# Optimization experiments

Measured on AMD Instinct MI355X. Metric: run time of the kernel, lower is better.

The kernel has to match this reference:

```python
import jax, jax.numpy as jnp
import numpy as np

NEG_SLOPE = 0.2


def setup_inputs() -> dict:
    key = jax.random.key(0)
    k1, k2, k3 = jax.random.split(key, 3)
    B, N, IN, OUT, C = 2048, 256, 256, 256, 1024
    x = jax.random.normal(k1, (B, N, IN), dtype=jnp.float32)
    indices = jax.random.randint(k2, (B,), 0, C)
    # kaiming-uniform-like init for weight
    bound = float(np.sqrt(6.0 / IN))
    weight = jax.random.uniform(k3, (C, IN, OUT), dtype=jnp.float32, minval=-bound, maxval=bound)
    bias = jnp.zeros((1, 1, OUT), dtype=jnp.float32)
    return {"x": x, "indices": indices, "weight": weight, "bias": bias}


def reference(x, indices, weight, bias):
    # gather per-batch weight tiles: [B, IN, OUT], then batched matmul
    w = weight[indices]                      # [B, IN, OUT]
    out = jnp.einsum('bni,bio->bno', x, w)   # [B, N, OUT]
    out = out + bias[0]                      # bias[0] is [1, OUT], broadcasts
    return jnp.where(out >= 0, out, NEG_SLOPE * out)  # LeakyReLU(0.2)
```

## Files before the change

kernel.cpp:

```cpp
#include <hip/hip_runtime.h>
#include <hip/hip_bf16.h>


#define N_DIM 256
#define K_DIM 256
#define O_DIM 256
#define BK 32

typedef __attribute__((ext_vector_type(8))) __bf16 bf16x8;
typedef __attribute__((ext_vector_type(4))) float f32x4;
typedef __attribute__((ext_vector_type(4))) unsigned int u32x4;
typedef __attribute__((ext_vector_type(2))) unsigned int u32x2;

__device__ __forceinline__ f32x4 MFMA(u32x4 a, u32x4 b, f32x4 c) {
    return __builtin_amdgcn_mfma_f32_16x16x32_bf16(
        __builtin_bit_cast(bf16x8, a), __builtin_bit_cast(bf16x8, b), c, 0, 0, 0);
}

__device__ __forceinline__ unsigned pk2(float a, float b) {
    __hip_bfloat16 ha = __float2bfloat16(a);
    __hip_bfloat16 hb = __float2bfloat16(b);
    unsigned short sa, sb;
    __builtin_memcpy(&sa, &ha, 2);
    __builtin_memcpy(&sb, &hb, 2);
    return (unsigned)sa | ((unsigned)sb << 16);
}

__device__ __forceinline__ int swz(int row, int k) {
    const int rp = row >> 1;
    const int ch = (((row & 1) << 2) + (k >> 3)) ^ (rp & 7);
    return rp * 128 + ch * 16 + (k & 7) * 2;
}

__global__ __launch_bounds__(256) void argemm_kernel(
    const float* __restrict__ x,
    const int* __restrict__ idx,
    const float* __restrict__ w,
    const float* __restrict__ bias,
    float* __restrict__ out)
{
    __shared__ __align__(16) char lds[32768];

    const int tid = threadIdx.x;
    const int l   = tid & 63;
    const int wid = tid >> 6;
    const int wr  = wid >> 1;
    const int wc  = wid & 1;

    const unsigned bid     = blockIdx.x;
    const unsigned chunk   = gridDim.x >> 3;
    const unsigned logical = (bid & 7u) * chunk + (bid >> 3);
    const int b    = (int)(logical >> 2);
    const int tpos = (int)(logical & 3u);
    const int n0   = (tpos >> 1) * 128;
    const int o0   = (tpos & 1) * 128;

    const int c = idx[b];
    const float* xb = x + (size_t)b * (N_DIM * K_DIM);
    const float* wb = w + (size_t)c * (K_DIM * O_DIM);

    const int lr3 = l >> 3, kc = l & 7;
    int gA[4], aW[4];
#pragma unroll
    for (int q = 0; q < 4; ++q) {
        const int rA = wid * 32 + q * 8 + lr3;
        gA[q] = (n0 + rA) * K_DIM + kc * 4;
        aW[q] = swz(rA, kc * 4);
    }
    const int kq = tid >> 5;
    const int m4 = (tid & 31) * 4;
    int gB[4], bW[4];
#pragma unroll
    for (int dk = 0; dk < 4; ++dk)
        gB[dk] = (kq * 4 + dk) * O_DIM + o0 + m4;
#pragma unroll
    for (int j = 0; j < 4; ++j)
        bW[j] = 16384 + swz(m4 + j, kq * 4);

    const int g = l >> 4;
    const int i = l & 15;
    int aR[4], bR[4];
#pragma unroll
    for (int m = 0; m < 4; ++m) aR[m] = swz(wr * 64 + m * 16 + i, g * 8);
#pragma unroll
    for (int n = 0; n < 4; ++n) bR[n] = 16384 + swz(wc * 64 + n * 16 + i, g * 8);

    f32x4 ra[4], rb[4];

    auto issue = [&](int t) {
#pragma unroll
        for (int q = 0; q < 4; ++q)
            ra[q] = *(const f32x4*)(xb + gA[q] + t * BK);
#pragma unroll
        for (int dk = 0; dk < 4; ++dk)
            rb[dk] = *(const f32x4*)(wb + gB[dk] + t * (BK * O_DIM));
    };
    auto flush = [&](int buf) {
        char* base = (char*)lds + buf * 8192;
#pragma unroll
        for (int q = 0; q < 4; ++q) {
            u32x2 p;
            p.x = pk2(ra[q].x, ra[q].y);
            p.y = pk2(ra[q].z, ra[q].w);
            *(u32x2*)(base + aW[q]) = p;
        }
#pragma unroll
        for (int j = 0; j < 4; ++j) {
            u32x2 p;
            p.x = pk2(rb[0][j], rb[1][j]);
            p.y = pk2(rb[2][j], rb[3][j]);
            *(u32x2*)(base + bW[j]) = p;
        }
    };

    f32x4 acc[4][4];
#pragma unroll
    for (int m = 0; m < 4; ++m)
#pragma unroll
        for (int n = 0; n < 4; ++n)
            acc[m][n] = (f32x4){0.f, 0.f, 0.f, 0.f};

    issue(0);
    flush(0);
    issue(1);
    asm volatile("s_waitcnt lgkmcnt(0)" ::: "memory");
    __builtin_amdgcn_sched_barrier(0);
    __builtin_amdgcn_s_barrier();

#pragma unroll
    for (int t = 0; t < 8; ++t) {
        const int cur = t & 1;
        const char* base = (const char*)lds + cur * 8192;

        u32x4 af[4];
#pragma unroll
        for (int m = 0; m < 4; ++m)
            af[m] = *(const u32x4*)(base + aR[m]);
#pragma unroll
        for (int n = 0; n < 4; ++n) {
            const u32x4 bq = *(const u32x4*)(base + bR[n]);
#pragma unroll
            for (int m = 0; m < 4; ++m)
                acc[m][n] = MFMA(af[m], bq, acc[m][n]);
        }

        if (t < 7) {
            flush(cur ^ 1);
            if (t < 6) issue(t + 2);
            asm volatile("s_waitcnt lgkmcnt(0)" ::: "memory");
            __builtin_amdgcn_sched_barrier(0);
            __builtin_amdgcn_s_barrier();
        }
    }

    float biasf[4];
#pragma unroll
    for (int n = 0; n < 4; ++n)
        biasf[n] = bias[o0 + wc * 64 + n * 16 + i];

    float* ob = out + (size_t)b * (N_DIM * O_DIM);
#pragma unroll
    for (int m = 0; m < 4; ++m) {
#pragma unroll
        for (int r = 0; r < 4; ++r) {
            const int row = n0 + wr * 64 + m * 16 + g * 4 + r;
#pragma unroll
            for (int n = 0; n < 4; ++n) {
                float v = acc[m][n][r] + biasf[n];
                v = (v >= 0.f) ? v : 0.2f * v;
                ob[row * O_DIM + o0 + wc * 64 + n * 16 + i] = v;
            }
        }
    }
}

extern "C" void kernel_launch(void* const* d_in, const int* in_sizes, int n_in,
                              void* d_out, int out_size, void* d_ws, size_t ws_size,
                              hipStream_t stream) {
    const float* x    = (const float*)d_in[0];
    const int*   idx  = (const int*)d_in[1];
    const float* w    = (const float*)d_in[2];
    const float* bias = (const float*)d_in[3];
    float*       out  = (float*)d_out;
    (void)d_ws; (void)ws_size; (void)n_in; (void)out_size;

    const int B = in_sizes[1];
    dim3 grid((unsigned)(B * 4)), block(256);
    hipLaunchKernelGGL(argemm_kernel, grid, block, 0, stream, x, idx, w, bias, out);
}
```

Baseline: 307.7 us.

## Load A fragments directly to registers and stage B in per-wave LDS

The x tile no longer goes through shared memory: each wave loads its A rows straight from global memory in MFMA fragment layout and packs them to bf16 in registers. The weight tile is staged in a private per-wave LDS double buffer with a new swizzle, so the block-wide barriers and lgkmcnt waits are removed. The aim is to drop barrier stalls and A-side LDS round trips. In exchange, A and B global loads are duplicated across the waves that previously shared them, which raises L2 traffic, and the A accesses coalesce less well.

```diff
diff --git a/kernel.cpp b/kernel.cpp
--- a/kernel.cpp
+++ b/kernel.cpp
@@ -5,12 +5,10 @@
 #define N_DIM 256
 #define K_DIM 256
 #define O_DIM 256
-#define BK 32
 
 typedef __attribute__((ext_vector_type(8))) __bf16 bf16x8;
 typedef __attribute__((ext_vector_type(4))) float f32x4;
 typedef __attribute__((ext_vector_type(4))) unsigned int u32x4;
-typedef __attribute__((ext_vector_type(2))) unsigned int u32x2;
 
 __device__ __forceinline__ f32x4 MFMA(u32x4 a, u32x4 b, f32x4 c) {
     return __builtin_amdgcn_mfma_f32_16x16x32_bf16(
@@ -24,12 +22,6 @@
     __builtin_memcpy(&sa, &ha, 2);
     __builtin_memcpy(&sb, &hb, 2);
     return (unsigned)sa | ((unsigned)sb << 16);
-}
-
-__device__ __forceinline__ int swz(int row, int k) {
-    const int rp = row >> 1;
-    const int ch = (((row & 1) << 2) + (k >> 3)) ^ (rp & 7);
-    return rp * 128 + ch * 16 + (k & 7) * 2;
 }
 
 __global__ __launch_bounds__(256) void argemm_kernel(
@@ -57,59 +49,51 @@
 
     const int c = idx[b];
     const float* xb = x + (size_t)b * (N_DIM * K_DIM);
-    const float* wb = w + (size_t)c * (K_DIM * O_DIM);
-
-    const int lr3 = l >> 3, kc = l & 7;
-    int gA[4], aW[4];
-#pragma unroll
-    for (int q = 0; q < 4; ++q) {
-        const int rA = wid * 32 + q * 8 + lr3;
-        gA[q] = (n0 + rA) * K_DIM + kc * 4;
-        aW[q] = swz(rA, kc * 4);
-    }
-    const int kq = tid >> 5;
-    const int m4 = (tid & 31) * 4;
-    int gB[4], bW[4];
-#pragma unroll
-    for (int dk = 0; dk < 4; ++dk)
-        gB[dk] = (kq * 4 + dk) * O_DIM + o0 + m4;
-#pragma unroll
-    for (int j = 0; j < 4; ++j)
-        bW[j] = 16384 + swz(m4 + j, kq * 4);
+    const float* wv = w + (size_t)c * (K_DIM * O_DIM) + o0 + wc * 64;
 
     const int g = l >> 4;
     const int i = l & 15;
-    int aR[4], bR[4];
+
+    char* const ldsw = (char*)lds + wid * 8192;
+    const int bR = (i >> 1) * 128 + ((g * 2 + (i & 1)) ^ ((i >> 1) & 7)) * 16;
+    int bW[4];
 #pragma unroll
-    for (int m = 0; m < 4; ++m) aR[m] = swz(wr * 64 + m * 16 + i, g * 8);
+    for (int j = 0; j < 4; ++j) {
+        const int orow = i * 4 + j;
+        bW[j] = (orow >> 1) * 128 + ((g * 2 + (orow & 1)) ^ ((orow >> 1) & 7)) * 16;
+    }
+
+    const float* xr[4];
 #pragma unroll
-    for (int n = 0; n < 4; ++n) bR[n] = 16384 + swz(wc * 64 + n * 16 + i, g * 8);
+    for (int m = 0; m < 4; ++m)
+        xr[m] = xb + (n0 + wr * 64 + m * 16 + i) * K_DIM + g * 8;
 
-    f32x4 ra[4], rb[4];
+    const float* wp = wv + (g * 8) * O_DIM + i * 4;
 
-    auto issue = [&](int t) {
+    f32x4 ra[8], rb[8];
+
+    auto issueA = [&](int t) {
 #pragma unroll
-        for (int q = 0; q < 4; ++q)
-            ra[q] = *(const f32x4*)(xb + gA[q] + t * BK);
+        for (int m = 0; m < 4; ++m) {
+            ra[2 * m]     = *(const f32x4*)(xr[m] + t * 32);
+            ra[2 * m + 1] = *(const f32x4*)(xr[m] + t * 32 + 4);
+        }
+    };
+    auto issueB = [&](int t) {
 #pragma unroll
-        for (int dk = 0; dk < 4; ++dk)
-            rb[dk] = *(const f32x4*)(wb + gB[dk] + t * (BK * O_DIM));
+        for (int dk = 0; dk < 8; ++dk)
+            rb[dk] = *(const f32x4*)(wp + (size_t)(t * 32 + dk) * O_DIM);
     };
-    auto flush = [&](int buf) {
-        char* base = (char*)lds + buf * 8192;
-#pragma unroll
-        for (int q = 0; q < 4; ++q) {
-            u32x2 p;
-            p.x = pk2(ra[q].x, ra[q].y);
-            p.y = pk2(ra[q].z, ra[q].w);
-            *(u32x2*)(base + aW[q]) = p;
-        }
+    auto flushB = [&](int buf) {
+        char* d = ldsw + buf * 4096;
 #pragma unroll
         for (int j = 0; j < 4; ++j) {
-            u32x2 p;
+            u32x4 p;
             p.x = pk2(rb[0][j], rb[1][j]);
             p.y = pk2(rb[2][j], rb[3][j]);
-            *(u32x2*)(base + bW[j]) = p;
+            p.z = pk2(rb[4][j], rb[5][j]);
+            p.w = pk2(rb[6][j], rb[7][j]);
+            *(u32x4*)(d + bW[j]) = p;
         }
     };
 
@@ -120,36 +104,36 @@
         for (int n = 0; n < 4; ++n)
             acc[m][n] = (f32x4){0.f, 0.f, 0.f, 0.f};
 
-    issue(0);
-    flush(0);
-    issue(1);
-    asm volatile("s_waitcnt lgkmcnt(0)" ::: "memory");
-    __builtin_amdgcn_sched_barrier(0);
-    __builtin_amdgcn_s_barrier();
+    issueB(0);
+    issueA(0);
+    flushB(0);
+    issueB(1);
 
 #pragma unroll
     for (int t = 0; t < 8; ++t) {
         const int cur = t & 1;
-        const char* base = (const char*)lds + cur * 8192;
 
         u32x4 af[4];
 #pragma unroll
-        for (int m = 0; m < 4; ++m)
-            af[m] = *(const u32x4*)(base + aR[m]);
+        for (int m = 0; m < 4; ++m) {
+            af[m].x = pk2(ra[2 * m].x,     ra[2 * m].y);
+            af[m].y = pk2(ra[2 * m].z,     ra[2 * m].w);
+            af[m].z = pk2(ra[2 * m + 1].x, ra[2 * m + 1].y);
+            af[m].w = pk2(ra[2 * m + 1].z, ra[2 * m + 1].w);
+        }
+        if (t < 7) {
+            issueA(t + 1);
+            flushB(cur ^ 1);
+        }
+        if (t < 6) issueB(t + 2);
+
+        const char* s = ldsw + cur * 4096;
 #pragma unroll
         for (int n = 0; n < 4; ++n) {
-            const u32x4 bq = *(const u32x4*)(base + bR[n]);
+            const u32x4 bq = *(const u32x4*)(s + bR + n * 1024);
 #pragma unroll
             for (int m = 0; m < 4; ++m)
                 acc[m][n] = MFMA(af[m], bq, acc[m][n]);
-        }
-
-        if (t < 7) {
-            flush(cur ^ 1);
-            if (t < 6) issue(t + 2);
-            asm volatile("s_waitcnt lgkmcnt(0)" ::: "memory");
-            __builtin_amdgcn_sched_barrier(0);
-            __builtin_amdgcn_s_barrier();
         }
     }
 
```

New measurement: 468.4 us. 52.2% more time.

## Deepen global-load prefetch to two tiles with triple-buffered LDS

Applied to the files above, without the earlier changes.

Keeps two sets of prefetch registers so global loads for tile t+3 are issued while tile t+1 is flushed. LDS becomes three 16 KB stages instead of two, with scheduling barriers around each issue. The aim is to hide more global memory latency for this memory-bound fp32-input GEMM. In exchange it uses more VGPRs for the extra in-flight registers and 48 KB of LDS per block, which may reduce occupancy. The LDS stages are sized larger than the 8 KB each tile needs.

```diff
diff --git a/kernel.cpp b/kernel.cpp
--- a/kernel.cpp
+++ b/kernel.cpp
@@ -39,7 +39,7 @@
     const float* __restrict__ bias,
     float* __restrict__ out)
 {
-    __shared__ __align__(16) char lds[32768];
+    __shared__ __align__(16) char lds[49152];
 
     const int tid = threadIdx.x;
     const int l   = tid & 63;
@@ -75,7 +75,7 @@
         gB[dk] = (kq * 4 + dk) * O_DIM + o0 + m4;
 #pragma unroll
     for (int j = 0; j < 4; ++j)
-        bW[j] = 16384 + swz(m4 + j, kq * 4);
+        bW[j] = swz(m4 + j, kq * 4);
 
     const int g = l >> 4;
     const int i = l & 15;
@@ -83,33 +83,33 @@
 #pragma unroll
     for (int m = 0; m < 4; ++m) aR[m] = swz(wr * 64 + m * 16 + i, g * 8);
 #pragma unroll
-    for (int n = 0; n < 4; ++n) bR[n] = 16384 + swz(wc * 64 + n * 16 + i, g * 8);
+    for (int n = 0; n < 4; ++n) bR[n] = 8192 + swz(wc * 64 + n * 16 + i, g * 8);
 
-    f32x4 ra[4], rb[4];
+    f32x4 ra[2][4], rb[2][4];
 
-    auto issue = [&](int t) {
+    auto issue = [&](int t, int s) {
 #pragma unroll
         for (int q = 0; q < 4; ++q)
-            ra[q] = *(const f32x4*)(xb + gA[q] + t * BK);
+            ra[s][q] = *(const f32x4*)(xb + gA[q] + t * BK);
 #pragma unroll
         for (int dk = 0; dk < 4; ++dk)
-            rb[dk] = *(const f32x4*)(wb + gB[dk] + t * (BK * O_DIM));
+            rb[s][dk] = *(const f32x4*)(wb + gB[dk] + t * (BK * O_DIM));
     };
-    auto flush = [&](int buf) {
-        char* base = (char*)lds + buf * 8192;
+    auto flush = [&](int t, int s) {
+        char* base = (char*)lds + (t % 3) * 16384;
 #pragma unroll
         for (int q = 0; q < 4; ++q) {
             u32x2 p;
-            p.x = pk2(ra[q].x, ra[q].y);
-            p.y = pk2(ra[q].z, ra[q].w);
+            p.x = pk2(ra[s][q].x, ra[s][q].y);
+            p.y = pk2(ra[s][q].z, ra[s][q].w);
             *(u32x2*)(base + aW[q]) = p;
         }
 #pragma unroll
         for (int j = 0; j < 4; ++j) {
             u32x2 p;
-            p.x = pk2(rb[0][j], rb[1][j]);
-            p.y = pk2(rb[2][j], rb[3][j]);
-            *(u32x2*)(base + bW[j]) = p;
+            p.x = pk2(rb[s][0][j], rb[s][1][j]);
+            p.y = pk2(rb[s][2][j], rb[s][3][j]);
+            *(u32x2*)(base + 8192 + bW[j]) = p;
         }
     };
 
@@ -120,17 +120,20 @@
         for (int n = 0; n < 4; ++n)
             acc[m][n] = (f32x4){0.f, 0.f, 0.f, 0.f};
 
-    issue(0);
-    flush(0);
-    issue(1);
+    issue(0, 0);
+    __builtin_amdgcn_sched_barrier(0);
+    issue(1, 1);
+    __builtin_amdgcn_sched_barrier(0);
+    flush(0, 0);
+    issue(2, 0);
+    __builtin_amdgcn_sched_barrier(0);
     asm volatile("s_waitcnt lgkmcnt(0)" ::: "memory");
     __builtin_amdgcn_sched_barrier(0);
     __builtin_amdgcn_s_barrier();
 
 #pragma unroll
     for (int t = 0; t < 8; ++t) {
-        const int cur = t & 1;
-        const char* base = (const char*)lds + cur * 8192;
+        const char* base = (const char*)lds + (t % 3) * 16384;
 
         u32x4 af[4];
 #pragma unroll
@@ -145,8 +148,11 @@
         }
 
         if (t < 7) {
-            flush(cur ^ 1);
-            if (t < 6) issue(t + 2);
+            flush(t + 1, (t + 1) & 1);
+            if (t < 5) {
+                issue(t + 3, (t + 1) & 1);
+                __builtin_amdgcn_sched_barrier(0);
+            }
             asm volatile("s_waitcnt lgkmcnt(0)" ::: "memory");
             __builtin_amdgcn_sched_barrier(0);
             __builtin_amdgcn_s_barrier();
```

Result: faster. 298.3 us (-3.1%).
